# Kernel tuning notes

Hardware: AMD Instinct MI355X
Metric: run time of the kernel (lower is better)

Reference implementation:

```python
import jax, jax.numpy as jnp
import numpy as np

MODEL_DIM = 4096
NH = 32          # query heads
NG = 8           # kv heads (query groups)
HD = MODEL_DIM // NH   # 128, == kv_head_dim in the module
KV_DIM = NG * HD       # 1024
BASE = 50000.0
B, S = 1, 2048


def setup_inputs() -> dict:
    key = jax.random.key(0)
    ks = jax.random.split(key, 3)
    s = 0.02
    return {
        "x": jax.random.normal(ks[0], (B, S, MODEL_DIM), jnp.float32),
        "Wqkv": jax.random.normal(ks[1], (MODEL_DIM, MODEL_DIM + 2 * KV_DIM), jnp.float32) * s,
        "bqkv": jnp.zeros((MODEL_DIM + 2 * KV_DIM,), jnp.float32),
        "Wo": jax.random.normal(ks[2], (MODEL_DIM, MODEL_DIM), jnp.float32) * s,
        "bo": jnp.zeros((MODEL_DIM,), jnp.float32),
    }


def _rope_tables(seq_len):
    # Llama-style RoPE: inv_freq over even dims, emb = concat(freqs, freqs)
    inv_freq = 1.0 / (BASE ** (jnp.arange(0, HD, 2, dtype=jnp.float32) / HD))
    t = jnp.arange(seq_len, dtype=jnp.float32)  # offset = 0 (no cache)
    freqs = t[:, None] * inv_freq[None, :]      # [S, HD/2]
    emb = jnp.concatenate([freqs, freqs], axis=-1)  # [S, HD]
    return jnp.cos(emb), jnp.sin(emb)


def _rotate_half(x):
    x1, x2 = jnp.split(x, 2, axis=-1)
    return jnp.concatenate([-x2, x1], axis=-1)


def reference(x, Wqkv, bqkv, Wo, bo):
    Bsz, Sl, _ = x.shape
    fused = x @ Wqkv + bqkv                                   # [B, S, D + 2*KV]
    q, k, v = jnp.split(fused, [MODEL_DIM, MODEL_DIM + KV_DIM], axis=-1)
    q = q.reshape(Bsz, Sl, NH, HD).transpose(0, 2, 1, 3)      # [B, NH, S, HD]
    k = k.reshape(Bsz, Sl, NG, HD).transpose(0, 2, 1, 3)      # [B, NG, S, HD]
    v = v.reshape(Bsz, Sl, NG, HD).transpose(0, 2, 1, 3)

    cos, sin = _rope_tables(Sl)                               # [S, HD] each
    q = q * cos + _rotate_half(q) * sin
    k = k * cos + _rotate_half(k) * sin

    # GQA without duplicating KV: group query heads per shared KV head
    G = NH // NG
    qg = q.reshape(Bsz, NG, G, Sl, HD)                        # [B, NG, G, S, HD]
    scale = 1.0 / jnp.sqrt(jnp.asarray(HD, q.dtype))
    scores = jnp.einsum('bngsd,bntd->bngst', qg, k) * scale   # [B, NG, G, S, S]
    causal = jnp.tril(jnp.ones((Sl, Sl), dtype=bool))
    scores = jnp.where(causal, scores, jnp.finfo(scores.dtype).min)
    attn = jax.nn.softmax(scores, axis=-1)
    out = jnp.einsum('bngst,bntd->bngsd', attn, v)            # [B, NG, G, S, HD]
    out = out.reshape(Bsz, NH, Sl, HD).transpose(0, 2, 1, 3).reshape(Bsz, Sl, MODEL_DIM)
    return out @ Wo + bo
```

## Files before the change

### kernel.cpp

```cpp
#include <hip/hip_runtime.h>
#include <hip/hip_bf16.h>
#include <math.h>

#define S_LEN  2048
#define MDIM   4096
#define NHEADS 32
#define NKV    8
#define HD     128
#define KVDIM  1024
#define NFUSED (MDIM + 2 * KVDIM)

typedef short bf16x8 __attribute__((ext_vector_type(8)));
typedef float f32x4 __attribute__((ext_vector_type(4)));
typedef float f32x16 __attribute__((ext_vector_type(16)));

__device__ __forceinline__ unsigned short f2b(float f) {
  union { float f; unsigned int u; } v; v.f = f;
  unsigned int r = v.u + 0x7FFFu + ((v.u >> 16) & 1u);
  return (unsigned short)(r >> 16);
}
__device__ __forceinline__ float b2f(unsigned short h) {
  union { unsigned int u; float f; } v; v.u = ((unsigned int)h) << 16;
  return v.f;
}

__device__ __forceinline__ void async_copy16(const void* g, void* l) {
  __builtin_amdgcn_global_load_lds(
      (const __attribute__((address_space(1))) unsigned int*)g,
      (__attribute__((address_space(3))) unsigned int*)l, 16, 0, 0);
}

__global__ __launch_bounds__(256) void prep_kernel(
    const float* __restrict__ x, const float* __restrict__ Wqkv,
    unsigned short* __restrict__ xb, float2* __restrict__ rtab,
    unsigned short* __restrict__ WT) {
  __shared__ float t[64 * 65];
  const int b = blockIdx.x;
  const int tid = threadIdx.x;

  if (b < 4096) {
    size_t i = (size_t)b * 256 + tid;
    const float4 a = ((const float4*)x)[2 * i];
    const float4 c = ((const float4*)x)[2 * i + 1];
    unsigned short o[8] = {f2b(a.x), f2b(a.y), f2b(a.z), f2b(a.w),
                           f2b(c.x), f2b(c.y), f2b(c.z), f2b(c.w)};
    *(int4*)(xb + 8 * i) = *(const int4*)o;
  } else if (b < 4608) {
    int idx = (b - 4096) * 256 + tid;
    int s = idx >> 6, d = idx & 63;
    float inv_freq = __expf(-0.16905903569f * (float)d);
    float ang = (float)s * inv_freq;
    rtab[idx] = make_float2(cosf(ang), sinf(ang));
  } else {
    const int tt = b - 4608;
    const int n0 = (tt % 96) << 6;
    const int k0 = (tt / 96) << 6;
    const int K = MDIM, N = NFUSED;
#pragma unroll
    for (int it = 0; it < 4; ++it) {
      int idx = it * 256 + tid;
      int r = idx >> 4;
      int cq = idx & 15;
      const float4 v =
          *(const float4*)(Wqkv + (size_t)(k0 + r) * N + n0 + (cq << 2));
      t[r * 65 + (cq << 2) + 0] = v.x;
      t[r * 65 + (cq << 2) + 1] = v.y;
      t[r * 65 + (cq << 2) + 2] = v.z;
      t[r * 65 + (cq << 2) + 3] = v.w;
    }
    __syncthreads();
    const int n = tid >> 2, kk = (tid & 3) << 4;
    unsigned short o[16];
#pragma unroll
    for (int j = 0; j < 16; ++j) o[j] = f2b(t[(kk + j) * 65 + n]);
    *(int4*)(WT + (size_t)(n0 + n) * K + k0 + kk) = *(const int4*)&o[0];
    *(int4*)(WT + (size_t)(n0 + n) * K + k0 + kk + 8) = *(const int4*)&o[8];
  }
}

__global__ __launch_bounds__(512, 2) void gemm1_kernel(
    const unsigned short* __restrict__ xb,
    const unsigned short* __restrict__ WT, const float* __restrict__ bias,
    const float2* __restrict__ rtab, unsigned short* __restrict__ Qb,
    unsigned short* __restrict__ Kb, unsigned short* __restrict__ Vt) {
  __shared__ unsigned short sm[2][32768];

  const int tid = threadIdx.x;
  const int bn = blockIdx.x, bm = blockIdx.y;
  const int lane = tid & 63, wave = tid >> 6;
  const int l31 = lane & 31, lh = lane >> 5;
  const int wrow = wave >> 2, wcol = wave & 3;

  f32x16 acc[4][2];
#pragma unroll
  for (int i = 0; i < 4; ++i)
#pragma unroll
    for (int j = 0; j < 2; ++j)
#pragma unroll
      for (int r = 0; r < 16; ++r) acc[i][j][r] = 0.f;

  const int lr8 = lane >> 3, lc8 = lane & 7;
  const int baser = wave * 8 + lr8;
  const size_t swz = (size_t)((lc8 ^ lr8 ^ wave) << 3);
  const unsigned short* sA = xb + (size_t)(bm * 256 + baser) * MDIM + swz;
  const unsigned short* sB = WT + (size_t)(bn * 256 + baser) * MDIM + swz;

  auto stage = [&](int slot, int k0) {
#pragma unroll
    for (int c = 0; c < 4; ++c) {
      unsigned short* dA = &sm[slot][(c * 64 + wave * 8) * 64];
      unsigned short* dB = &sm[slot][16384 + (c * 64 + wave * 8) * 64];
      async_copy16(sA + (size_t)c * 64 * MDIM + k0, dA);
      async_copy16(sB + (size_t)c * 64 * MDIM + k0, dB);
    }
  };

  const int arow0 = wrow * 128 + l31;
  const int brow0 = wcol * 64 + l31;
  const int base = (l31 & 7) ^ (l31 >> 3);

  stage(0, 0);

  for (int kt = 0; kt < 64; ++kt) {
    const int p = kt & 1;
    asm volatile("s_waitcnt vmcnt(0)" ::: "memory");
    __builtin_amdgcn_s_barrier();
    __builtin_amdgcn_sched_barrier(0);

    if (kt < 63) stage(p ^ 1, (kt + 1) << 6);

    const unsigned short* Asl = &sm[p][0];
    const unsigned short* Bsl = &sm[p][16384];
    __builtin_amdgcn_s_setprio(1);
#pragma unroll
    for (int t = 0; t < 4; ++t) {
      const int coE = (((2 * t + lh) ^ base) << 3);
      const int coO = coE ^ 32;
      bf16x8 bfr[2], af[4];
      bfr[0] = *(const bf16x8*)&Bsl[(brow0) * 64 + coE];
      bfr[1] = *(const bf16x8*)&Bsl[(brow0 + 32) * 64 + coO];
      af[0] = *(const bf16x8*)&Asl[(arow0) * 64 + coE];
      af[1] = *(const bf16x8*)&Asl[(arow0 + 32) * 64 + coO];
      af[2] = *(const bf16x8*)&Asl[(arow0 + 64) * 64 + coE];
      af[3] = *(const bf16x8*)&Asl[(arow0 + 96) * 64 + coO];
#pragma unroll
      for (int i = 0; i < 4; ++i)
#pragma unroll
        for (int jj = 0; jj < 2; ++jj)
          acc[i][jj] = __builtin_amdgcn_mfma_f32_32x32x16_bf16(
              af[i], bfr[jj], acc[i][jj], 0, 0, 0);
    }
    __builtin_amdgcn_s_setprio(0);
  }
  __syncthreads();

  unsigned short* Ct = &sm[0][0];
#pragma unroll 1
  for (int h = 0; h < 2; ++h) {
    const int slot = 2 * bn + h;
    if ((wcol >> 1) == h) {
#pragma unroll
      for (int i = 0; i < 4; ++i)
#pragma unroll
        for (int jj = 0; jj < 2; ++jj) {
          int lc = (wcol & 1) * 64 + jj * 32 + l31;
          float bv = bias[slot * 128 + lc];
#pragma unroll
          for (int r = 0; r < 16; ++r) {
            int lrw = wrow * 128 + i * 32 + (r & 3) + 8 * (r >> 2) + 4 * lh;
            Ct[lrw * 132 + lc] = f2b(acc[i][jj][r] + bv);
          }
        }
    }
    __syncthreads();

    if (slot < 40) {
#pragma unroll 4
      for (int it = 0; it < 32; ++it) {
        int row = it * 8 + wave;
        int d = lane;
        float x1 = b2f(Ct[row * 132 + d]);
        float x2 = b2f(Ct[row * 132 + d + 64]);
        int s = bm * 256 + row;
        float2 cs = rtab[s * 64 + d];
        float o1 = x1 * cs.x - x2 * cs.y;
        float o2 = x2 * cs.x + x1 * cs.y;
        unsigned short* dst;
        if (slot < 32)
          dst = Qb + ((size_t)slot * S_LEN + s) * HD;
        else
          dst = Kb + ((size_t)(slot - 32) * S_LEN + s) * HD;
        dst[d] = f2b(o1);
        dst[d + 64] = f2b(o2);
      }
    } else {
      const int g = slot - 40;
      unsigned short* Vtg = Vt + (size_t)g * HD * S_LEN;
      const int dp = tid >> 3;
      const int sq = (tid & 7) << 5;
      unsigned short buf0[32], buf1[32];
#pragma unroll
      for (int i = 0; i < 32; ++i) {
        unsigned int w = *(const unsigned int*)&Ct[(sq + i) * 132 + 2 * dp];
        buf0[i] = (unsigned short)(w & 0xffffu);
        buf1[i] = (unsigned short)(w >> 16);
      }
      const int s0 = bm * 256 + sq;
#pragma unroll
      for (int c = 0; c < 2; ++c) {
        unsigned short* dst = Vtg + (size_t)(2 * dp + c) * S_LEN + s0;
        const unsigned short* b = c ? buf1 : buf0;
#pragma unroll
        for (int q4 = 0; q4 < 4; ++q4)
          *(int4*)(dst + q4 * 8) = *(const int4*)(b + q4 * 8);
      }
    }
    __syncthreads();
  }
}

__global__ __launch_bounds__(512, 2) void gemm2_kernel(
    const unsigned short* __restrict__ Ab16,
    const unsigned short* __restrict__ BT, const float* __restrict__ bias,
    float* __restrict__ C) {
  __shared__ unsigned short sm[2][24576];

  const int tid = threadIdx.x;
  const int bn = blockIdx.x, bm = blockIdx.y;
  const int lane = tid & 63, wave = tid >> 6;
  const int l31 = lane & 31, lh = lane >> 5;
  const int wrow = wave >> 2, wcol = wave & 3;

  f32x16 acc[2][2];
#pragma unroll
  for (int i = 0; i < 2; ++i)
#pragma unroll
    for (int j = 0; j < 2; ++j)
#pragma unroll
      for (int r = 0; r < 16; ++r) acc[i][j][r] = 0.f;

  const int lr8 = lane >> 3, lc8 = lane & 7;
  const int baser = wave * 8 + lr8;
  const size_t swz = (size_t)((lc8 ^ lr8 ^ wave) << 3);
  const unsigned short* sA = Ab16 + (size_t)(bm * 128 + baser) * MDIM + swz;
  const unsigned short* sB = BT + (size_t)(bn * 256 + baser) * MDIM + swz;

  auto stage = [&](int slot, int k0) {
#pragma unroll
    for (int c = 0; c < 2; ++c)
      async_copy16(sA + (size_t)c * 64 * MDIM + k0,
                   &sm[slot][(c * 64 + wave * 8) * 64]);
#pragma unroll
    for (int c = 0; c < 4; ++c)
      async_copy16(sB + (size_t)c * 64 * MDIM + k0,
                   &sm[slot][8192 + (c * 64 + wave * 8) * 64]);
  };

  const int arow0 = wrow * 64 + l31;
  const int brow0 = wcol * 64 + l31;
  const int base = (l31 & 7) ^ (l31 >> 3);

  stage(0, 0);

#pragma unroll 1
  for (int kt = 0; kt < 64; ++kt) {
    const int p = kt & 1;
    asm volatile("s_waitcnt vmcnt(0)" ::: "memory");
    __builtin_amdgcn_s_barrier();
    __builtin_amdgcn_sched_barrier(0);

    if (kt < 63) stage(p ^ 1, (kt + 1) << 6);

    const unsigned short* Asl = &sm[p][0];
    const unsigned short* Bsl = &sm[p][8192];
    __builtin_amdgcn_s_setprio(1);
#pragma unroll
    for (int t = 0; t < 4; ++t) {
      const int coE = (((2 * t + lh) ^ base) << 3);
      const int coO = coE ^ 32;
      bf16x8 bfr[2], af[2];
      bfr[0] = *(const bf16x8*)&Bsl[(brow0) * 64 + coE];
      bfr[1] = *(const bf16x8*)&Bsl[(brow0 + 32) * 64 + coO];
      af[0] = *(const bf16x8*)&Asl[(arow0) * 64 + coE];
      af[1] = *(const bf16x8*)&Asl[(arow0 + 32) * 64 + coO];
#pragma unroll
      for (int i = 0; i < 2; ++i)
#pragma unroll
        for (int jj = 0; jj < 2; ++jj)
          acc[i][jj] = __builtin_amdgcn_mfma_f32_32x32x16_bf16(
              af[i], bfr[jj], acc[i][jj], 0, 0, 0);
    }
    __builtin_amdgcn_s_setprio(0);
  }

#pragma unroll
  for (int i = 0; i < 2; ++i)
#pragma unroll
    for (int jj = 0; jj < 2; ++jj) {
      int gcol = bn * 256 + wcol * 64 + jj * 32 + l31;
      float bv = bias[gcol];
#pragma unroll
      for (int r = 0; r < 16; ++r) {
        int grow =
            bm * 128 + wrow * 64 + i * 32 + (r & 3) + 8 * (r >> 2) + 4 * lh;
        C[(size_t)grow * MDIM + gcol] = acc[i][jj][r] + bv;
      }
    }
}

__device__ __forceinline__ void stage_kv(const unsigned short* __restrict__ Kg,
                                         const unsigned short* __restrict__ Vg,
                                         int jtile, unsigned short* KsBuf,
                                         unsigned short* VsBuf, int wv,
                                         int lane) {
  const unsigned short* kg = Kg + (size_t)jtile * 64 * HD;
  const unsigned short* vg = Vg + jtile * 64;
#pragma unroll
  for (int it = 0; it < 4; ++it) {
    int kr = wv * 16 + it * 4 + (lane >> 4);
    async_copy16(kg + (size_t)kr * HD + (((lane & 15) ^ (kr & 7)) << 3),
                 KsBuf + (wv * 16 + it * 4) * 128);
    int vr = wv * 32 + it * 8 + (lane >> 3);
    async_copy16(vg + (size_t)vr * S_LEN + (((lane & 7) ^ (vr & 7)) << 3),
                 VsBuf + (wv * 32 + it * 8) * 64);
  }
}

__global__ __launch_bounds__(256, 2) void flash_kernel(
    const unsigned short* __restrict__ Qb, const unsigned short* __restrict__ Kb,
    const unsigned short* __restrict__ Vt, unsigned short* __restrict__ attnb,
    const float* __restrict__ Wo, unsigned short* __restrict__ WoT) {
  __shared__ __align__(16) unsigned short Ks[2][64 * 128];
  __shared__ __align__(16) unsigned short Vs[2][128 * 64];
  __shared__ __align__(16) unsigned short Ps[64 * 72];

  const int tid = threadIdx.x;
  const int bid = blockIdx.x;

  if (bid >= 1024) {
    float* t = (float*)&Ks[0][0];
    const int tt = bid - 1024;
    const int n0 = (tt & 63) << 6;
    const int k0 = (tt >> 6) << 6;
#pragma unroll
    for (int it = 0; it < 4; ++it) {
      int idx = it * 256 + tid;
      int r = idx >> 4;
      int cq = idx & 15;
      const float4 v =
          *(const float4*)(Wo + (size_t)(k0 + r) * MDIM + n0 + (cq << 2));
      t[r * 65 + (cq << 2) + 0] = v.x;
      t[r * 65 + (cq << 2) + 1] = v.y;
      t[r * 65 + (cq << 2) + 2] = v.z;
      t[r * 65 + (cq << 2) + 3] = v.w;
    }
    __syncthreads();
    const int n = tid >> 2, kk = (tid & 3) << 4;
    unsigned short o[16];
#pragma unroll
    for (int j = 0; j < 16; ++j) o[j] = f2b(t[(kk + j) * 65 + n]);
    *(int4*)(WoT + (size_t)(n0 + n) * MDIM + k0 + kk) = *(const int4*)&o[0];
    *(int4*)(WoT + (size_t)(n0 + n) * MDIM + k0 + kk + 8) =
        *(const int4*)&o[8];
    return;
  }

  const int h = bid & 31;
  const int qt = 31 - (bid >> 5);
  const int g = h >> 2;
  const int wv = tid >> 6, lane = tid & 63;
  const int lrow = lane & 15, quad = lane >> 4;
  const float scale = 0.08838834764831845f;

  const unsigned short* Qg = Qb + ((size_t)h * S_LEN + qt * 64) * HD;
  bf16x8 qf[4];
#pragma unroll
  for (int ks = 0; ks < 4; ++ks)
    qf[ks] = *(const bf16x8*)(Qg + (size_t)(wv * 16 + lrow) * HD + ks * 32 +
                              quad * 8);

  bf16x8 ones;
#pragma unroll
  for (int i = 0; i < 8; ++i) ones[i] = (short)0x3F80;

  const unsigned short* Kg = Kb + (size_t)g * S_LEN * HD;
  const unsigned short* Vg = Vt + (size_t)g * HD * S_LEN;

  f32x4 l_acc = {0.f, 0.f, 0.f, 0.f};
  f32x4 o_acc[8];
#pragma unroll
  for (int jc = 0; jc < 8; ++jc) {
    f32x4 z = {0.f, 0.f, 0.f, 0.f};
    o_acc[jc] = z;
  }

  stage_kv(Kg, Vg, 0, &Ks[0][0], &Vs[0][0], wv, lane);

  for (int jt = 0; jt <= qt; ++jt) {
    const int cb = jt & 1;
    asm volatile("s_waitcnt vmcnt(0)" ::: "memory");
    __builtin_amdgcn_s_barrier();
    __builtin_amdgcn_sched_barrier(0);

    if (jt < qt)
      stage_kv(Kg, Vg, jt + 1, &Ks[cb ^ 1][0], &Vs[cb ^ 1][0], wv, lane);

    f32x4 s_acc[4];
#pragma unroll
    for (int j = 0; j < 4; ++j) {
      f32x4 z = {0.f, 0.f, 0.f, 0.f};
      s_acc[j] = z;
    }
#pragma unroll
    for (int ks = 0; ks < 4; ++ks)
#pragma unroll
      for (int j = 0; j < 4; ++j) {
        int row = j * 16 + lrow;
        bf16x8 bk = *(const bf16x8*)&Ks[cb][row * 128 +
                                           (((ks * 4 + quad) ^ (row & 7)) << 3)];
        s_acc[j] = __builtin_amdgcn_mfma_f32_16x16x32_bf16(qf[ks], bk,
                                                           s_acc[j], 0, 0, 0);
      }

    if (jt == qt) {
#pragma unroll
      for (int r = 0; r < 4; ++r) {
        int grow = qt * 64 + wv * 16 + quad * 4 + r;
#pragma unroll
        for (int j = 0; j < 4; ++j) {
          int gcol = jt * 64 + j * 16 + lrow;
          float p =
              (gcol <= grow) ? __expf(s_acc[j][r] * scale - 12.0f) : 0.f;
          Ps[(wv * 16 + quad * 4 + r) * 72 + j * 16 + lrow] = f2b(p);
        }
      }
    } else {
#pragma unroll
      for (int r = 0; r < 4; ++r)
#pragma unroll
        for (int j = 0; j < 4; ++j) {
          float p = __expf(s_acc[j][r] * scale - 12.0f);
          Ps[(wv * 16 + quad * 4 + r) * 72 + j * 16 + lrow] = f2b(p);
        }
    }
    asm volatile("s_waitcnt lgkmcnt(0)" ::: "memory");
    __builtin_amdgcn_sched_barrier(0);

#pragma unroll
    for (int kk = 0; kk < 2; ++kk) {
      bf16x8 ap =
          *(const bf16x8*)&Ps[(wv * 16 + lrow) * 72 + kk * 32 + 8 * quad];
      l_acc = __builtin_amdgcn_mfma_f32_16x16x32_bf16(ap, ones, l_acc, 0, 0, 0);
#pragma unroll
      for (int jc = 0; jc < 8; ++jc) {
        int row = jc * 16 + lrow;
        bf16x8 bv = *(const bf16x8*)&Vs[cb][row * 64 +
                                            (((kk * 4 + quad) ^ (row & 7)) << 3)];
        o_acc[jc] = __builtin_amdgcn_mfma_f32_16x16x32_bf16(ap, bv, o_acc[jc],
                                                            0, 0, 0);
      }
    }
    __builtin_amdgcn_s_barrier();
  }

#pragma unroll
  for (int r = 0; r < 4; ++r) {
    float inv_l = 1.0f / l_acc[r];
    int row = qt * 64 + wv * 16 + quad * 4 + r;
#pragma unroll
    for (int jc = 0; jc < 8; ++jc) {
      int col = jc * 16 + lrow;
      attnb[(size_t)row * MDIM + h * HD + col] = f2b(o_acc[jc][r] * inv_l);
    }
  }
}

extern "C" void kernel_launch(void* const* d_in, const int* in_sizes, int n_in,
                              void* d_out, int out_size, void* d_ws,
                              size_t ws_size, hipStream_t stream) {
  const float* x = (const float*)d_in[0];
  const float* Wqkv = (const float*)d_in[1];
  const float* bqkv = (const float*)d_in[2];
  const float* Wo = (const float*)d_in[3];
  const float* bo = (const float*)d_in[4];
  float* out = (float*)d_out;

  unsigned char* ws = (unsigned char*)d_ws;
  unsigned short* WT = (unsigned short*)ws;
  unsigned short* WoT = (unsigned short*)ws;
  unsigned short* attnb = (unsigned short*)(ws + 33554432);
  unsigned short* Qb = (unsigned short*)(ws + 50331648);
  unsigned short* Kb = (unsigned short*)(ws + 67108864);
  unsigned short* Vt = (unsigned short*)(ws + 71303168);
  unsigned short* xb = (unsigned short*)d_out;
  float2* rtab = (float2*)((unsigned char*)d_out + 16777216);

  prep_kernel<<<4096 + 512 + 6144, 256, 0, stream>>>(x, Wqkv, xb, rtab, WT);
  gemm1_kernel<<<dim3(NFUSED / 256, S_LEN / 256), 512, 0, stream>>>(
      xb, WT, bqkv, rtab, Qb, Kb, Vt);
  flash_kernel<<<1024 + 4096, 256, 0, stream>>>(Qb, Kb, Vt, attnb, Wo, WoT);
  gemm2_kernel<<<dim3(MDIM / 256, S_LEN / 128), 512, 0, stream>>>(attnb, WoT,
                                                                  bo, out);
}
```

Before: 458.0 us.

## Double query tile per flash block to reuse K/V tiles, drop double buffering

Each flash attention block now handles 128 query rows (two 16-row subtiles per wave) instead of 64, so every staged K/V tile feeds twice as many MFMAs and the number of attention blocks is halved. Shared memory is cut to a single K/V buffer, and the next tile is no longer prefetched during compute; loads are issued and waited on at the top of each iteration. This lowers K/V global traffic and LDS footprint but exposes load latency and doubles accumulator register pressure, which may reduce occupancy. Causal work per block also becomes coarser, and the diagonal masking now covers two tiles.

```diff
diff --git a/kernel.cpp b/kernel.cpp
--- a/kernel.cpp
+++ b/kernel.cpp
@@ -330,16 +330,17 @@
     const unsigned short* __restrict__ Qb, const unsigned short* __restrict__ Kb,
     const unsigned short* __restrict__ Vt, unsigned short* __restrict__ attnb,
     const float* __restrict__ Wo, unsigned short* __restrict__ WoT) {
-  __shared__ __align__(16) unsigned short Ks[2][64 * 128];
-  __shared__ __align__(16) unsigned short Vs[2][128 * 64];
-  __shared__ __align__(16) unsigned short Ps[64 * 72];
+  __shared__ __align__(16) unsigned short smem[25600];
+  unsigned short* Ks = smem;
+  unsigned short* Vs = smem + 8192;
+  unsigned short* Ps = smem + 16384;
 
   const int tid = threadIdx.x;
   const int bid = blockIdx.x;
 
-  if (bid >= 1024) {
-    float* t = (float*)&Ks[0][0];
-    const int tt = bid - 1024;
+  if (bid >= 512) {
+    float* t = (float*)smem;
+    const int tt = bid - 512;
     const int n0 = (tt & 63) << 6;
     const int k0 = (tt >> 6) << 6;
 #pragma unroll
@@ -366,18 +367,21 @@
   }
 
   const int h = bid & 31;
-  const int qt = 31 - (bid >> 5);
+  const int qt = 15 - (bid >> 5);
   const int g = h >> 2;
   const int wv = tid >> 6, lane = tid & 63;
   const int lrow = lane & 15, quad = lane >> 4;
   const float scale = 0.08838834764831845f;
 
-  const unsigned short* Qg = Qb + ((size_t)h * S_LEN + qt * 64) * HD;
-  bf16x8 qf[4];
-#pragma unroll
-  for (int ks = 0; ks < 4; ++ks)
-    qf[ks] = *(const bf16x8*)(Qg + (size_t)(wv * 16 + lrow) * HD + ks * 32 +
-                              quad * 8);
+  const unsigned short* Qg = Qb + ((size_t)h * S_LEN + qt * 128) * HD;
+  bf16x8 qf[2][4];
+#pragma unroll
+  for (int rt = 0; rt < 2; ++rt)
+#pragma unroll
+    for (int ks = 0; ks < 4; ++ks)
+      qf[rt][ks] = *(const bf16x8*)(Qg +
+                                    (size_t)(wv * 32 + rt * 16 + lrow) * HD +
+                                    ks * 32 + quad * 8);
 
   bf16x8 ones;
 #pragma unroll
@@ -386,93 +390,111 @@
   const unsigned short* Kg = Kb + (size_t)g * S_LEN * HD;
   const unsigned short* Vg = Vt + (size_t)g * HD * S_LEN;
 
-  f32x4 l_acc = {0.f, 0.f, 0.f, 0.f};
-  f32x4 o_acc[8];
-#pragma unroll
-  for (int jc = 0; jc < 8; ++jc) {
+  f32x4 l_acc[2];
+  f32x4 o_acc[2][8];
+#pragma unroll
+  for (int rt = 0; rt < 2; ++rt) {
     f32x4 z = {0.f, 0.f, 0.f, 0.f};
-    o_acc[jc] = z;
-  }
-
-  stage_kv(Kg, Vg, 0, &Ks[0][0], &Vs[0][0], wv, lane);
-
-  for (int jt = 0; jt <= qt; ++jt) {
-    const int cb = jt & 1;
+    l_acc[rt] = z;
+#pragma unroll
+    for (int jc = 0; jc < 8; ++jc) o_acc[rt][jc] = z;
+  }
+
+  const int ntiles = 2 * qt + 2;
+  for (int jt = 0; jt < ntiles; ++jt) {
+    stage_kv(Kg, Vg, jt, Ks, Vs, wv, lane);
     asm volatile("s_waitcnt vmcnt(0)" ::: "memory");
     __builtin_amdgcn_s_barrier();
     __builtin_amdgcn_sched_barrier(0);
 
-    if (jt < qt)
-      stage_kv(Kg, Vg, jt + 1, &Ks[cb ^ 1][0], &Vs[cb ^ 1][0], wv, lane);
-
-    f32x4 s_acc[4];
-#pragma unroll
-    for (int j = 0; j < 4; ++j) {
-      f32x4 z = {0.f, 0.f, 0.f, 0.f};
-      s_acc[j] = z;
-    }
+    f32x4 s_acc[2][4];
+#pragma unroll
+    for (int rt = 0; rt < 2; ++rt)
+#pragma unroll
+      for (int j = 0; j < 4; ++j) {
+        f32x4 z = {0.f, 0.f, 0.f, 0.f};
+        s_acc[rt][j] = z;
+      }
 #pragma unroll
     for (int ks = 0; ks < 4; ++ks)
 #pragma unroll
       for (int j = 0; j < 4; ++j) {
         int row = j * 16 + lrow;
-        bf16x8 bk = *(const bf16x8*)&Ks[cb][row * 128 +
-                                           (((ks * 4 + quad) ^ (row & 7)) << 3)];
-        s_acc[j] = __builtin_amdgcn_mfma_f32_16x16x32_bf16(qf[ks], bk,
-                                                           s_acc[j], 0, 0, 0);
-      }
-
-    if (jt == qt) {
-#pragma unroll
-      for (int r = 0; r < 4; ++r) {
-        int grow = qt * 64 + wv * 16 + quad * 4 + r;
-#pragma unroll
-        for (int j = 0; j < 4; ++j) {
-          int gcol = jt * 64 + j * 16 + lrow;
-          float p =
-              (gcol <= grow) ? __expf(s_acc[j][r] * scale - 12.0f) : 0.f;
-          Ps[(wv * 16 + quad * 4 + r) * 72 + j * 16 + lrow] = f2b(p);
+        bf16x8 bk = *(const bf16x8*)&Ks[row * 128 +
+                                        (((ks * 4 + quad) ^ (row & 7)) << 3)];
+        s_acc[0][j] = __builtin_amdgcn_mfma_f32_16x16x32_bf16(
+            qf[0][ks], bk, s_acc[0][j], 0, 0, 0);
+        s_acc[1][j] = __builtin_amdgcn_mfma_f32_16x16x32_bf16(
+            qf[1][ks], bk, s_acc[1][j], 0, 0, 0);
+      }
+
+    if (jt >= 2 * qt) {
+#pragma unroll
+      for (int rt = 0; rt < 2; ++rt)
+#pragma unroll
+        for (int r = 0; r < 4; ++r) {
+          int grow = qt * 128 + wv * 32 + rt * 16 + quad * 4 + r;
+#pragma unroll
+          for (int j = 0; j < 4; ++j) {
+            int gcol = jt * 64 + j * 16 + lrow;
+            float p =
+                (gcol <= grow) ? __expf(s_acc[rt][j][r] * scale - 12.0f) : 0.f;
+            Ps[(wv * 32 + rt * 16 + quad * 4 + r) * 72 + j * 16 + lrow] =
+                f2b(p);
+          }
         }
-      }
     } else {
 #pragma unroll
-      for (int r = 0; r < 4; ++r)
-#pragma unroll
-        for (int j = 0; j < 4; ++j) {
-          float p = __expf(s_acc[j][r] * scale - 12.0f);
-          Ps[(wv * 16 + quad * 4 + r) * 72 + j * 16 + lrow] = f2b(p);
-        }
+      for (int rt = 0; rt < 2; ++rt)
+#pragma unroll
+        for (int r = 0; r < 4; ++r)
+#pragma unroll
+          for (int j = 0; j < 4; ++j) {
+            float p = __expf(s_acc[rt][j][r] * scale - 12.0f);
+            Ps[(wv * 32 + rt * 16 + quad * 4 + r) * 72 + j * 16 + lrow] =
+                f2b(p);
+          }
     }
     asm volatile("s_waitcnt lgkmcnt(0)" ::: "memory");
     __builtin_amdgcn_sched_barrier(0);
 
 #pragma unroll
     for (int kk = 0; kk < 2; ++kk) {
-      bf16x8 ap =
-          *(const bf16x8*)&Ps[(wv * 16 + lrow) * 72 + kk * 32 + 8 * quad];
-      l_acc = __builtin_amdgcn_mfma_f32_16x16x32_bf16(ap, ones, l_acc, 0, 0, 0);
+      bf16x8 ap0 = *(const bf16x8*)&Ps[(wv * 32 + lrow) * 72 + kk * 32 +
+                                       8 * quad];
+      bf16x8 ap1 = *(const bf16x8*)&Ps[(wv * 32 + 16 + lrow) * 72 + kk * 32 +
+                                       8 * quad];
+      l_acc[0] =
+          __builtin_amdgcn_mfma_f32_16x16x32_bf16(ap0, ones, l_acc[0], 0, 0, 0);
+      l_acc[1] =
+          __builtin_amdgcn_mfma_f32_16x16x32_bf16(ap1, ones, l_acc[1], 0, 0, 0);
 #pragma unroll
       for (int jc = 0; jc < 8; ++jc) {
         int row = jc * 16 + lrow;
-        bf16x8 bv = *(const bf16x8*)&Vs[cb][row * 64 +
-                                            (((kk * 4 + quad) ^ (row & 7)) << 3)];
-        o_acc[jc] = __builtin_amdgcn_mfma_f32_16x16x32_bf16(ap, bv, o_acc[jc],
-                                                            0, 0, 0);
+        bf16x8 bv = *(const bf16x8*)&Vs[row * 64 +
+                                        (((kk * 4 + quad) ^ (row & 7)) << 3)];
+        o_acc[0][jc] = __builtin_amdgcn_mfma_f32_16x16x32_bf16(
+            ap0, bv, o_acc[0][jc], 0, 0, 0);
+        o_acc[1][jc] = __builtin_amdgcn_mfma_f32_16x16x32_bf16(
+            ap1, bv, o_acc[1][jc], 0, 0, 0);
       }
     }
     __builtin_amdgcn_s_barrier();
   }
 
 #pragma unroll
-  for (int r = 0; r < 4; ++r) {
-    float inv_l = 1.0f / l_acc[r];
-    int row = qt * 64 + wv * 16 + quad * 4 + r;
-#pragma unroll
-    for (int jc = 0; jc < 8; ++jc) {
-      int col = jc * 16 + lrow;
-      attnb[(size_t)row * MDIM + h * HD + col] = f2b(o_acc[jc][r] * inv_l);
-    }
-  }
+  for (int rt = 0; rt < 2; ++rt)
+#pragma unroll
+    for (int r = 0; r < 4; ++r) {
+      float inv_l = 1.0f / l_acc[rt][r];
+      int row = qt * 128 + wv * 32 + rt * 16 + quad * 4 + r;
+#pragma unroll
+      for (int jc = 0; jc < 8; ++jc) {
+        int col = jc * 16 + lrow;
+        attnb[(size_t)row * MDIM + h * HD + col] =
+            f2b(o_acc[rt][jc][r] * inv_l);
+      }
+    }
 }
 
 extern "C" void kernel_launch(void* const* d_in, const int* in_sizes, int n_in,
@@ -498,7 +520,7 @@
   prep_kernel<<<4096 + 512 + 6144, 256, 0, stream>>>(x, Wqkv, xb, rtab, WT);
   gemm1_kernel<<<dim3(NFUSED / 256, S_LEN / 256), 512, 0, stream>>>(
       xb, WT, bqkv, rtab, Qb, Kb, Vt);
-  flash_kernel<<<1024 + 4096, 256, 0, stream>>>(Qb, Kb, Vt, attnb, Wo, WoT);
+  flash_kernel<<<512 + 4096, 256, 0, stream>>>(Qb, Kb, Vt, attnb, Wo, WoT);
   gemm2_kernel<<<dim3(MDIM / 256, S_LEN / 128), 512, 0, stream>>>(attnb, WoT,
                                                                   bo, out);
 }
```

After: 457.7 us. Within noise of the previous version (-0.1%).
